# Performance work log

Measured on AMD Instinct MI355X. Metric: run time of the kernel, lower is better.

## Reference

```python
import jax, jax.numpy as jnp
import numpy as np

N = 32768       # batch of received vectors
N_RX = 8        # real-valued rx dimension (rows of G)
N_TX = 4        # n_tx_re
N_SYM = 4       # n_sym_re
K = N_SYM ** N_TX  # 256 joint symbol combos
SYMS = np.array([-3.0, -1.0, 1.0, 3.0]) / np.sqrt(5.0)  # 16-QAM real levels


def setup_inputs() -> dict:
    key = jax.random.key(0)
    k1, k2, k3, k4 = jax.random.split(key, 4)
    log_qi = jax.random.normal(k1, (N, N_TX, N_SYM), dtype=jnp.float32)
    G = jax.random.normal(k2, (N, N_RX, N_TX), dtype=jnp.float32)
    sqrt_2rho = jax.random.uniform(k3, (N,), dtype=jnp.float32, minval=0.5, maxval=2.0)
    n_var = jax.random.uniform(k4, (N,), dtype=jnp.float32, minval=0.05, maxval=0.5)
    # alpha is a NonNeg scalar weight (constant-initialized to 1.0). We use 0.8
    # (a plausible post-training value) so the (1-alpha)*log_qi path is exercised.
    alpha = jnp.float32(0.8)
    return {"log_qi": log_qi, "G": G, "sqrt_2rho": sqrt_2rho, "n_var": n_var, "alpha": alpha}


def _laplace_log_cdf(x):
    # Laplace(0,1): cdf = 0.5*exp(x) for x<0, 1 - 0.5*exp(-x) for x>=0
    return jnp.where(x < 0, x - jnp.log(2.0), jnp.log1p(-0.5 * jnp.exp(-jnp.abs(x))))


def reference(log_qi, G, sqrt_2rho, n_var, alpha):
    dt = log_qi.dtype
    syms = jnp.asarray(SYMS, dtype=dt)
    # All K = N_SYM**N_TX joint index combos (meshgrid 'ij' order = self.s_map order)
    grids = jnp.meshgrid(*([jnp.arange(N_SYM)] * N_TX), indexing='ij')
    idx = jnp.stack([g.reshape(-1) for g in grids], axis=-1)   # (K, N_TX) int
    s_all = syms[idx]                                          # (K, N_TX)

    # log p(y | s) for every joint combo: shared by all N_TX updates
    sG = sqrt_2rho[:, None, None] * G                          # (N, N_RX, N_TX)
    term = jnp.einsum('brt,kt->brk', sG, s_all)                # (N, N_RX, K)
    log_p = jnp.sum(_laplace_log_cdf(term), axis=1)            # (N, K)

    tx_ids = jnp.arange(N_TX)
    for xi in range(N_TX):  # unrolled Python loop, as in the original
        qi_un = jnp.exp(log_qi)
        qi = qi_un / jnp.sum(qi_un, axis=-1, keepdims=True)    # compute_qi
        # qi gathered at each combo: qi_sel[b,k,j] = qi[b, j, idx[k,j]]
        qi_sel = qi[:, tx_ids, idx]                            # (N, K, N_TX)
        # product over j != xi (row xi replaced by 1.0, as in tf.where insert)
        w = jnp.prod(jnp.where(tx_ids == xi, jnp.asarray(1.0, dt), qi_sel), axis=-1)  # (N, K)
        # group-sum combos by their xi-th symbol index
        onehot = (idx[:, xi][:, None] == jnp.arange(N_SYM)).astype(dt)  # (K, N_SYM)
        ex_log_qi = (w * log_p) @ onehot                       # (N, N_SYM)
        new_row = (1.0 - alpha) * log_qi[:, xi, :] + alpha * jax.lax.stop_gradient(ex_log_qi)
        log_qi = log_qi.at[:, xi, :].set(new_row)
        log_qi = log_qi - jax.lax.stop_gradient(jnp.max(log_qi, axis=-1, keepdims=True))
    return log_qi
```

## Files before the change

### kernel.cpp

```cpp
#include <hip/hip_runtime.h>

#define LOG2E 1.4426950408889634f
#define LN2F  0.6931471805599453f
#define RS5F  0.4472135954999579f

template<int XOR, int OR, int AND>
__device__ __forceinline__ float swz(float v) {
    return __int_as_float(__builtin_amdgcn_ds_swizzle(
        __float_as_int(v), (XOR << 10) | (OR << 5) | AND));
}
#define SWZX(v, m) swz<(m), 0, 0x1F>(v)
#define EXP2(x)  __builtin_amdgcn_exp2f(x)
#define LOG2_(x) __builtin_amdgcn_logf(x)
#define RCP_(x)  __builtin_amdgcn_rcpf(x)

__device__ __forceinline__ float bperm(int byte_addr, float v) {
    return __int_as_float(__builtin_amdgcn_ds_bpermute(byte_addr, __float_as_int(v)));
}

__device__ __forceinline__ float sel4(float e0, float e1, float e2, float e3, int c) {
    float lo = (c & 1) ? e1 : e0;
    float hi = (c & 1) ? e3 : e2;
    return (c & 2) ? hi : lo;
}

__global__ __launch_bounds__(256, 8) void mfnet_layer_kernel(
    const float* __restrict__ log_qi,
    const float* __restrict__ G,
    const float* __restrict__ sqrt_2rho,
    const float* __restrict__ alpha_ptr,
    float* __restrict__ out,
    int N)
{
    const int tid  = threadIdx.x;
    const int wv   = tid >> 6;
    const int lane = tid & 63;
    const int grp  = lane >> 5;
    const int u    = lane & 31;
    const int ib   = blockIdx.x * 8 + wv * 2;

    __shared__ __align__(16) float sG[4][64];
    {
        size_t gidx = (size_t)ib * 32 + (size_t)lane;
        size_t gmax = (size_t)N * 32 - 1;
        if (gidx > gmax) gidx = gmax;
        sG[wv][lane] = G[gidx];
    }

    const int it0   = ib + grp;
    const bool valid = (it0 < N);
    const int item  = valid ? it0 : (N - 1);

    const float alpha = alpha_ptr[0];
    const float alm1  = 1.0f - alpha;

    const int bit0 = u & 1;
    const int c2   = (u >> 1) & 3;
    const int c1   = (u >> 3) & 3;
    const int ue   = u & 15;
    const int row  = ue >> 2;
    const int col  = ue & 3;

    const float rv = sqrt_2rho[item] * (RS5F * LOG2E);
    const float s1 = rv * (float)(2 * c1 - 3);
    const float s2 = rv * (float)(2 * c2 - 3);
    const float w0 = rv * (float)(2 * bit0 - 3);

    float slqD = log_qi[(size_t)item * 16 + ue] * LOG2E;
    {
        float m1 = fmaxf(slqD, SWZX(slqD, 1));
        float m  = fmaxf(m1, SWZX(m1, 2));
        slqD -= m;
    }

    auto softmax_all = [&](float s) {
        float e = EXP2(s);
        float t = e + SWZX(e, 1);
        float den = t + SWZX(t, 2);
        return e * RCP_(den);
    };
    float qD = softmax_all(slqD);

    const int gbase = lane & 32;
    const int aQ1A = (gbase + 4 + c1) << 2;
    const int aQ1C = (gbase + 4 + (c1 ^ 3)) << 2;
    const int aQ2A = (gbase + 8 + c2) << 2;
    const int aQ2C = (gbase + 8 + (c2 ^ 3)) << 2;
    const int aR1  = (gbase + (col << 3)) << 2;
    const int aR2  = (gbase + (col << 1)) << 2;

    float q1A = bperm(aQ1A, qD), q1C = bperm(aQ1C, qD);
    float q2A = bperm(aQ2A, qD), q2C = bperm(aQ2C, qD);
    const int a3 = (gbase + 12) << 2;
    float q3v0 = bperm(a3, qD),      q3v1 = bperm(a3 + 4, qD);
    float q3v2 = bperm(a3 + 8, qD),  q3v3 = bperm(a3 + 12, qD);

    float lpA[4] = {0, 0, 0, 0};
    float lpC[4] = {0, 0, 0, 0};
    const float* gw = &sG[wv][grp * 32];
#pragma unroll
    for (int r = 0; r < 8; ++r) {
        float4 g = *(const float4*)(gw + r * 4);
        float tb = fmaf(g.x, w0, fmaf(g.y, s1, g.z * s2));
        float m3 = g.w * rv;
#pragma unroll
        for (int j = 0; j < 4; ++j) {
            float t  = fmaf(m3, (float)(2 * j - 3), tb);
            float at = -fabsf(t);
            float e  = EXP2(at);
            float lg = LOG2_(fmaf(e, -0.5f, 1.0f));
            float ng = at - 1.0f;
            bool neg = (t < 0.0f);
            lpA[j] += neg ? ng : lg;
            lpC[j] += neg ? lg : ng;
        }
    }

    float UA = lpA[0]*q3v0 + lpA[1]*q3v1 + lpA[2]*q3v2 + lpA[3]*q3v3;
    float UC = lpC[0]*q3v3 + lpC[1]*q3v2 + lpC[2]*q3v1 + lpC[3]*q3v0;

    float q0A, q0C, IA, IC;
    {
        float SA = UA * (q1A * q2A);
        float SC = UC * (q1C * q2C);
        SA += SWZX(SA,2); SA += SWZX(SA,4); SA += SWZX(SA,8); SA += SWZX(SA,16);
        SC += SWZX(SC,2); SC += SWZX(SC,4); SC += SWZX(SC,8); SC += SWZX(SC,16);
        float SAo = SWZX(SA, 1), SCo = SWZX(SC, 1);
        float A0 = bit0 ? SAo : SA;
        float A1 = bit0 ? SA  : SAo;
        float C1 = bit0 ? SC  : SCo;
        float C0 = bit0 ? SCo : SC;
        float exD = sel4(A0, A1, C1, C0, col);
        float bl = fmaf(alm1, slqD, alpha * exD);
        slqD = (row == 0) ? bl : slqD;
        float m1 = fmaxf(slqD, SWZX(slqD, 1));
        float m  = fmaxf(m1, SWZX(m1, 2));
        slqD -= m;
        qD = softmax_all(slqD);
        q0A = bperm((gbase + bit0) << 2, qD);
        q0C = bperm((gbase + (bit0 ^ 3)) << 2, qD);
        IA = q0A * UA;
        IC = q0C * UC;
    }

    {
        float SA = q2A * IA, SC = q2C * IC;
        SA += SWZX(SA,1); SA += SWZX(SA,2); SA += SWZX(SA,4);
        SC += SWZX(SC,1); SC += SWZX(SC,2); SC += SWZX(SC,4);
        float T = SA + SWZX(SC, 24);
        float exD = bperm(aR1, T);
        float bl = fmaf(alm1, slqD, alpha * exD);
        slqD = (row == 1) ? bl : slqD;
        float m1 = fmaxf(slqD, SWZX(slqD, 1));
        float m  = fmaxf(m1, SWZX(m1, 2));
        slqD -= m;
        qD = softmax_all(slqD);
        q1A = bperm(aQ1A, qD); q1C = bperm(aQ1C, qD);
    }

    {
        float SA = q1A * IA, SC = q1C * IC;
        SA += SWZX(SA,1); SA += SWZX(SA,8); SA += SWZX(SA,16);
        SC += SWZX(SC,1); SC += SWZX(SC,8); SC += SWZX(SC,16);
        float T = SA + SWZX(SC, 6);
        float exD = bperm(aR2, T);
        float bl = fmaf(alm1, slqD, alpha * exD);
        slqD = (row == 2) ? bl : slqD;
        float m1 = fmaxf(slqD, SWZX(slqD, 1));
        float m  = fmaxf(m1, SWZX(m1, 2));
        slqD -= m;
        qD = softmax_all(slqD);
        q2A = bperm(aQ2A, qD); q2C = bperm(aQ2C, qD);
    }

    {
        float WA = q0A * (q1A * q2A);
        float WC = q0C * (q1C * q2C);
        float R0 = lpA[0]*WA + lpC[3]*WC;
        float R1 = lpA[1]*WA + lpC[2]*WC;
        float R2 = lpA[2]*WA + lpC[1]*WC;
        float R3 = lpA[3]*WA + lpC[0]*WC;
        R0 += SWZX(R0,1); R0 += SWZX(R0,2); R0 += SWZX(R0,4); R0 += SWZX(R0,8); R0 += SWZX(R0,16);
        R1 += SWZX(R1,1); R1 += SWZX(R1,2); R1 += SWZX(R1,4); R1 += SWZX(R1,8); R1 += SWZX(R1,16);
        R2 += SWZX(R2,1); R2 += SWZX(R2,2); R2 += SWZX(R2,4); R2 += SWZX(R2,8); R2 += SWZX(R2,16);
        R3 += SWZX(R3,1); R3 += SWZX(R3,2); R3 += SWZX(R3,4); R3 += SWZX(R3,8); R3 += SWZX(R3,16);
        float exD = sel4(R0, R1, R2, R3, col);
        float bl = fmaf(alm1, slqD, alpha * exD);
        slqD = (row == 3) ? bl : slqD;
        float m1 = fmaxf(slqD, SWZX(slqD, 1));
        float m  = fmaxf(m1, SWZX(m1, 2));
        slqD -= m;
    }

    if (valid && u < 16) {
        out[(size_t)item * 16 + ue] = slqD * LN2F;
    }
}

extern "C" void kernel_launch(void* const* d_in, const int* in_sizes, int n_in,
                              void* d_out, int out_size, void* d_ws, size_t ws_size,
                              hipStream_t stream) {
    const float* log_qi = (const float*)d_in[0];
    const float* G      = (const float*)d_in[1];
    const float* rho    = (const float*)d_in[2];
    const float* alpha  = (const float*)d_in[4];
    float* out = (float*)d_out;

    const int N = in_sizes[2];
    const int blocks = (N + 7) / 8;
    mfnet_layer_kernel<<<blocks, 256, 0, stream>>>(log_qi, G, rho, alpha, out, N);
}
```

Before: 79.38 us.

## Map four items per wavefront with 16 lanes each, doubling per-lane combos

Each item now uses 16 lanes instead of 32, and each lane evaluates 8 symbol combos instead of 4. That halves the lanes spent per item and doubles the items handled per block. The post-loop reductions are restructured around the 16-lane group: several ds_bpermute gathers become ds_swizzle broadcasts, and the intermediate max-subtractions before each softmax are dropped. G is staged in shared memory with padded rows and float2 loads, and the launch bound is relaxed to 7 waves per SIMD, trading more registers per lane for less redundant transcendental work.

New measurement: 76.32 us. -3.9%, faster.

```diff
diff --git a/kernel.cpp b/kernel.cpp
--- a/kernel.cpp
+++ b/kernel.cpp
@@ -18,13 +18,7 @@
     return __int_as_float(__builtin_amdgcn_ds_bpermute(byte_addr, __float_as_int(v)));
 }
 
-__device__ __forceinline__ float sel4(float e0, float e1, float e2, float e3, int c) {
-    float lo = (c & 1) ? e1 : e0;
-    float hi = (c & 1) ? e3 : e2;
-    return (c & 2) ? hi : lo;
-}
-
-__global__ __launch_bounds__(256, 8) void mfnet_layer_kernel(
+__global__ __launch_bounds__(256, 7) void mfnet_layer_kernel(
     const float* __restrict__ log_qi,
     const float* __restrict__ G,
     const float* __restrict__ sqrt_2rho,
@@ -35,38 +29,34 @@
     const int tid  = threadIdx.x;
     const int wv   = tid >> 6;
     const int lane = tid & 63;
-    const int grp  = lane >> 5;
-    const int u    = lane & 31;
-    const int ib   = blockIdx.x * 8 + wv * 2;
-
-    __shared__ __align__(16) float sG[4][64];
-    {
-        size_t gidx = (size_t)ib * 32 + (size_t)lane;
-        size_t gmax = (size_t)N * 32 - 1;
+    const int grp  = (lane >> 4) & 3;
+    const int u    = lane & 15;
+    const int ib   = blockIdx.x * 16 + wv * 4;
+
+    __shared__ __align__(16) float sG[4][160];
+    {
+        size_t gidx = (size_t)ib * 32 + (size_t)(lane * 2);
+        size_t gmax = (size_t)N * 32 - 2;
         if (gidx > gmax) gidx = gmax;
-        sG[wv][lane] = G[gidx];
-    }
-
-    const int it0   = ib + grp;
+        float2 gv = *(const float2*)(G + gidx);
+        *(float2*)&sG[wv][grp * 40 + u * 2] = gv;
+    }
+
+    const int it0    = ib + grp;
     const bool valid = (it0 < N);
-    const int item  = valid ? it0 : (N - 1);
+    const int item   = valid ? it0 : (N - 1);
 
     const float alpha = alpha_ptr[0];
     const float alm1  = 1.0f - alpha;
 
-    const int bit0 = u & 1;
-    const int c2   = (u >> 1) & 3;
-    const int c1   = (u >> 3) & 3;
-    const int ue   = u & 15;
-    const int row  = ue >> 2;
-    const int col  = ue & 3;
+    const int col = u & 3;
+    const int row = u >> 2;
 
     const float rv = sqrt_2rho[item] * (RS5F * LOG2E);
-    const float s1 = rv * (float)(2 * c1 - 3);
-    const float s2 = rv * (float)(2 * c2 - 3);
-    const float w0 = rv * (float)(2 * bit0 - 3);
-
-    float slqD = log_qi[(size_t)item * 16 + ue] * LOG2E;
+    const float s1 = rv * (float)(2 * row - 3);
+    const float s2 = rv * (float)(2 * col - 3);
+
+    float slqD = log_qi[(size_t)item * 16 + u] * LOG2E;
     {
         float m1 = fmaxf(slqD, SWZX(slqD, 1));
         float m  = fmaxf(m1, SWZX(m1, 2));
@@ -74,38 +64,41 @@
     }
 
     auto softmax_all = [&](float s) {
-        float e = EXP2(s);
-        float t = e + SWZX(e, 1);
+        float e   = EXP2(s);
+        float t   = e + SWZX(e, 1);
         float den = t + SWZX(t, 2);
         return e * RCP_(den);
     };
     float qD = softmax_all(slqD);
 
-    const int gbase = lane & 32;
-    const int aQ1A = (gbase + 4 + c1) << 2;
-    const int aQ1C = (gbase + 4 + (c1 ^ 3)) << 2;
-    const int aQ2A = (gbase + 8 + c2) << 2;
-    const int aQ2C = (gbase + 8 + (c2 ^ 3)) << 2;
-    const int aR1  = (gbase + (col << 3)) << 2;
-    const int aR2  = (gbase + (col << 1)) << 2;
+    const int gb   = (lane & 0x30) << 2;
+    const int aQ1A = gb + ((4 + row) << 2);
+    const int aQ1C = gb + ((4 + (row ^ 3)) << 2);
+    const int aR1  = gb + (col << 4);
 
     float q1A = bperm(aQ1A, qD), q1C = bperm(aQ1C, qD);
-    float q2A = bperm(aQ2A, qD), q2C = bperm(aQ2C, qD);
-    const int a3 = (gbase + 12) << 2;
-    float q3v0 = bperm(a3, qD),      q3v1 = bperm(a3 + 4, qD);
-    float q3v2 = bperm(a3 + 8, qD),  q3v3 = bperm(a3 + 12, qD);
-
-    float lpA[4] = {0, 0, 0, 0};
-    float lpC[4] = {0, 0, 0, 0};
-    const float* gw = &sG[wv][grp * 32];
+    float q2A  = swz<0, 8, 0x13>(qD);
+    float q2C  = swz<3, 8, 0x13>(qD);
+    float q3v0 = swz<0, 12, 0x10>(qD);
+    float q3v1 = swz<0, 13, 0x10>(qD);
+    float q3v2 = swz<0, 14, 0x10>(qD);
+    float q3v3 = swz<0, 15, 0x10>(qD);
+
+    float lpA[8] = {0,0,0,0,0,0,0,0};
+    float lpC[8] = {0,0,0,0,0,0,0,0};
+    const float* gw = &sG[wv][grp * 40];
 #pragma unroll
     for (int r = 0; r < 8; ++r) {
-        float4 g = *(const float4*)(gw + r * 4);
-        float tb = fmaf(g.x, w0, fmaf(g.y, s1, g.z * s2));
-        float m3 = g.w * rv;
+        float4 g  = *(const float4*)(gw + r * 4);
+        float b12 = fmaf(g.y, s1, g.z * s2);
+        float m0  = g.x * rv;
+        float m3  = g.w * rv;
+        float t0  = fmaf(m0, -3.0f, b12);
+        float t1  = b12 - m0;
 #pragma unroll
-        for (int j = 0; j < 4; ++j) {
-            float t  = fmaf(m3, (float)(2 * j - 3), tb);
+        for (int j = 0; j < 8; ++j) {
+            float tb = (j & 4) ? t1 : t0;
+            float t  = fmaf(m3, (float)(2 * (j & 3) - 3), tb);
             float at = -fabsf(t);
             float e  = EXP2(at);
             float lg = LOG2_(fmaf(e, -0.5f, 1.0f));
@@ -116,84 +109,89 @@
         }
     }
 
-    float UA = lpA[0]*q3v0 + lpA[1]*q3v1 + lpA[2]*q3v2 + lpA[3]*q3v3;
-    float UC = lpC[0]*q3v3 + lpC[1]*q3v2 + lpC[2]*q3v1 + lpC[3]*q3v0;
-
-    float q0A, q0C, IA, IC;
-    {
-        float SA = UA * (q1A * q2A);
-        float SC = UC * (q1C * q2C);
-        SA += SWZX(SA,2); SA += SWZX(SA,4); SA += SWZX(SA,8); SA += SWZX(SA,16);
-        SC += SWZX(SC,2); SC += SWZX(SC,4); SC += SWZX(SC,8); SC += SWZX(SC,16);
-        float SAo = SWZX(SA, 1), SCo = SWZX(SC, 1);
-        float A0 = bit0 ? SAo : SA;
-        float A1 = bit0 ? SA  : SAo;
-        float C1 = bit0 ? SC  : SCo;
-        float C0 = bit0 ? SCo : SC;
-        float exD = sel4(A0, A1, C1, C0, col);
+    float UA0 = lpA[0]*q3v0 + lpA[1]*q3v1 + lpA[2]*q3v2 + lpA[3]*q3v3;
+    float UA1 = lpA[4]*q3v0 + lpA[5]*q3v1 + lpA[6]*q3v2 + lpA[7]*q3v3;
+    float UC3 = lpC[0]*q3v3 + lpC[1]*q3v2 + lpC[2]*q3v1 + lpC[3]*q3v0;
+    float UC2 = lpC[4]*q3v3 + lpC[5]*q3v2 + lpC[6]*q3v1 + lpC[7]*q3v0;
+
+    float JA, JC, Pin0, Pin1, Pin2, Pin3, Qin0, Qin1, Qin2, Qin3;
+    {
+        float preQ  = q1A * q2A;
+        float preQC = q1C * q2C;
+        float VA0 = UA0 * preQ,  VA1 = UA1 * preQ;
+        float VC2 = UC2 * preQC, VC3 = UC3 * preQC;
+        bool bb = (u & 1);
+        float S01 = (bb ? VA1 : VA0) + SWZX(bb ? VA0 : VA1, 1);
+        float S23 = (bb ? VC3 : VC2) + SWZX(bb ? VC2 : VC3, 1);
+        S01 += SWZX(S01, 2); S01 += SWZX(S01, 4); S01 += SWZX(S01, 8);
+        S23 += SWZX(S23, 2); S23 += SWZX(S23, 4); S23 += SWZX(S23, 8);
+        float exD = (col & 2) ? S23 : S01;
         float bl = fmaf(alm1, slqD, alpha * exD);
         slqD = (row == 0) ? bl : slqD;
+        qD = softmax_all(slqD);
+        float q0v0 = swz<0, 0, 0x10>(qD);
+        float q0v1 = swz<0, 1, 0x10>(qD);
+        float q0v2 = swz<0, 2, 0x10>(qD);
+        float q0v3 = swz<0, 3, 0x10>(qD);
+        JA = q0v0*UA0 + q0v1*UA1;
+        JC = q0v3*UC3 + q0v2*UC2;
+        Pin0 = lpA[0]*q0v0 + lpA[4]*q0v1;
+        Pin1 = lpA[1]*q0v0 + lpA[5]*q0v1;
+        Pin2 = lpA[2]*q0v0 + lpA[6]*q0v1;
+        Pin3 = lpA[3]*q0v0 + lpA[7]*q0v1;
+        Qin0 = lpC[3]*q0v3 + lpC[7]*q0v2;
+        Qin1 = lpC[2]*q0v3 + lpC[6]*q0v2;
+        Qin2 = lpC[1]*q0v3 + lpC[5]*q0v2;
+        Qin3 = lpC[0]*q0v3 + lpC[4]*q0v2;
+    }
+
+    {
+        float SA = q2A * JA, SC = q2C * JC;
+        SA += SWZX(SA, 1); SA += SWZX(SA, 2);
+        SC += SWZX(SC, 1); SC += SWZX(SC, 2);
+        float T = SA + SWZX(SC, 12);
+        float exD = bperm(aR1, T);
+        float bl = fmaf(alm1, slqD, alpha * exD);
+        slqD = (row == 1) ? bl : slqD;
+        qD = softmax_all(slqD);
+        q1A = bperm(aQ1A, qD); q1C = bperm(aQ1C, qD);
+    }
+
+    {
+        float SA = q1A * JA, SC = q1C * JC;
+        SA += SWZX(SA, 4); SA += SWZX(SA, 8);
+        SC += SWZX(SC, 4); SC += SWZX(SC, 8);
+        float exD = SA + SWZX(SC, 3);
+        float bl = fmaf(alm1, slqD, alpha * exD);
+        slqD = (row == 2) ? bl : slqD;
+        qD = softmax_all(slqD);
+        q2A = swz<0, 8, 0x13>(qD);
+        q2C = swz<3, 8, 0x13>(qD);
+    }
+
+    {
+        float WA = q1A * q2A, WC = q1C * q2C;
+        float V0 = Pin0*WA + Qin0*WC;
+        float V1 = Pin1*WA + Qin1*WC;
+        float V2 = Pin2*WA + Qin2*WC;
+        float V3 = Pin3*WA + Qin3*WC;
+        bool bb = (u & 1);
+        float S01 = (bb ? V1 : V0) + SWZX(bb ? V0 : V1, 1);
+        float S23 = (bb ? V3 : V2) + SWZX(bb ? V2 : V3, 1);
+        S01 += SWZX(S01, 2); S01 += SWZX(S01, 4); S01 += SWZX(S01, 8);
+        S23 += SWZX(S23, 2); S23 += SWZX(S23, 4); S23 += SWZX(S23, 8);
+        float exD = (col & 2) ? S23 : S01;
+        float bl = fmaf(alm1, slqD, alpha * exD);
+        slqD = (row == 3) ? bl : slqD;
+    }
+
+    {
         float m1 = fmaxf(slqD, SWZX(slqD, 1));
         float m  = fmaxf(m1, SWZX(m1, 2));
         slqD -= m;
-        qD = softmax_all(slqD);
-        q0A = bperm((gbase + bit0) << 2, qD);
-        q0C = bperm((gbase + (bit0 ^ 3)) << 2, qD);
-        IA = q0A * UA;
-        IC = q0C * UC;
-    }
-
-    {
-        float SA = q2A * IA, SC = q2C * IC;
-        SA += SWZX(SA,1); SA += SWZX(SA,2); SA += SWZX(SA,4);
-        SC += SWZX(SC,1); SC += SWZX(SC,2); SC += SWZX(SC,4);
-        float T = SA + SWZX(SC, 24);
-        float exD = bperm(aR1, T);
-        float bl = fmaf(alm1, slqD, alpha * exD);
-        slqD = (row == 1) ? bl : slqD;
-        float m1 = fmaxf(slqD, SWZX(slqD, 1));
-        float m  = fmaxf(m1, SWZX(m1, 2));
-        slqD -= m;
-        qD = softmax_all(slqD);
-        q1A = bperm(aQ1A, qD); q1C = bperm(aQ1C, qD);
-    }
-
-    {
-        float SA = q1A * IA, SC = q1C * IC;
-        SA += SWZX(SA,1); SA += SWZX(SA,8); SA += SWZX(SA,16);
-        SC += SWZX(SC,1); SC += SWZX(SC,8); SC += SWZX(SC,16);
-        float T = SA + SWZX(SC, 6);
-        float exD = bperm(aR2, T);
-        float bl = fmaf(alm1, slqD, alpha * exD);
-        slqD = (row == 2) ? bl : slqD;
-        float m1 = fmaxf(slqD, SWZX(slqD, 1));
-        float m  = fmaxf(m1, SWZX(m1, 2));
-        slqD -= m;
-        qD = softmax_all(slqD);
-        q2A = bperm(aQ2A, qD); q2C = bperm(aQ2C, qD);
-    }
-
-    {
-        float WA = q0A * (q1A * q2A);
-        float WC = q0C * (q1C * q2C);
-        float R0 = lpA[0]*WA + lpC[3]*WC;
-        float R1 = lpA[1]*WA + lpC[2]*WC;
-        float R2 = lpA[2]*WA + lpC[1]*WC;
-        float R3 = lpA[3]*WA + lpC[0]*WC;
-        R0 += SWZX(R0,1); R0 += SWZX(R0,2); R0 += SWZX(R0,4); R0 += SWZX(R0,8); R0 += SWZX(R0,16);
-        R1 += SWZX(R1,1); R1 += SWZX(R1,2); R1 += SWZX(R1,4); R1 += SWZX(R1,8); R1 += SWZX(R1,16);
-        R2 += SWZX(R2,1); R2 += SWZX(R2,2); R2 += SWZX(R2,4); R2 += SWZX(R2,8); R2 += SWZX(R2,16);
-        R3 += SWZX(R3,1); R3 += SWZX(R3,2); R3 += SWZX(R3,4); R3 += SWZX(R3,8); R3 += SWZX(R3,16);
-        float exD = sel4(R0, R1, R2, R3, col);
-        float bl = fmaf(alm1, slqD, alpha * exD);
-        slqD = (row == 3) ? bl : slqD;
-        float m1 = fmaxf(slqD, SWZX(slqD, 1));
-        float m  = fmaxf(m1, SWZX(m1, 2));
-        slqD -= m;
-    }
-
-    if (valid && u < 16) {
-        out[(size_t)item * 16 + ue] = slqD * LN2F;
+    }
+    if (valid) {
+        out[(size_t)item * 16 + u] = slqD * LN2F;
     }
 }
 
@@ -207,6 +205,6 @@
     float* out = (float*)d_out;
 
     const int N = in_sizes[2];
-    const int blocks = (N + 7) / 8;
+    const int blocks = (N + 15) / 16;
     mfnet_layer_kernel<<<blocks, 256, 0, stream>>>(log_qi, G, rho, alpha, out, N);
 }
```
